# Kernel tuning notes

Measured on AMD Instinct MI355X. Metric: run time of the kernel, lower is better.

The kernel has to match this reference:

```python
import jax, jax.numpy as jnp
import numpy as np

B, T, C, H = 4, 2048, 1024, 16
D = C // H  # head_dim = 64
ROPE_BASE = 10000.0
EPS = 1e-6


def _rms_norm(x):
    return x / jnp.sqrt(jnp.mean(x * x, axis=-1, keepdims=True) + EPS)


def _rope_tables(t_len, d, dtype):
    inv_freq = 1.0 / (ROPE_BASE ** (jnp.arange(0, d, 2, dtype=jnp.float32) / d))
    t = jnp.arange(t_len, dtype=jnp.float32)
    freqs = jnp.outer(t, inv_freq)  # [T, D/2]
    return jnp.cos(freqs).astype(dtype)[None, None], jnp.sin(freqs).astype(dtype)[None, None]


def _apply_rotary(x, cos, sin):
    d = x.shape[-1] // 2
    x1, x2 = x[..., :d], x[..., d:]
    return jnp.concatenate([x1 * cos + x2 * sin, -x1 * sin + x2 * cos], axis=-1)


def setup_inputs() -> dict:
    key = jax.random.key(0)
    k1, k2, k3, k4, k5 = jax.random.split(key, 5)
    x = jax.random.normal(k1, (B, T, C), dtype=jnp.float32)
    Wqkv = jax.random.normal(k2, (C, 3 * C), dtype=jnp.float32) * 0.02
    bqkv = jax.random.normal(k3, (3 * C,), dtype=jnp.float32) * 0.02
    # NOTE: original zero-inits c_proj.weight; randomized here for a non-trivial baseline.
    Wproj = jax.random.normal(k4, (C, C), dtype=jnp.float32) * 0.02
    bproj = jax.random.normal(k5, (C,), dtype=jnp.float32) * 0.02
    lamb = jnp.float32(0.5)
    return {"x": x, "Wqkv": Wqkv, "bqkv": bqkv, "Wproj": Wproj, "bproj": bproj, "lamb": lamb}


def reference(x, Wqkv, bqkv, Wproj, bproj, lamb):
    b, t, c = x.shape
    qkv = x @ Wqkv + bqkv  # [B,T,3C]
    q, k, v = jnp.split(qkv, 3, axis=-1)
    # [B,T,C] -> [B,H,T,D]
    to_heads = lambda z: z.reshape(b, t, H, D).transpose(0, 2, 1, 3)
    query, key_, value = to_heads(q), to_heads(k), to_heads(v)
    # v1 defaults to value -> blend is identity, kept for faithfulness
    value = (1.0 - lamb) * value + lamb * value
    query = _rms_norm(query)
    key_ = _rms_norm(key_)
    cos, sin = _rope_tables(t, D, x.dtype)
    query = _apply_rotary(query, cos, sin)
    key_ = _apply_rotary(key_, cos, sin)
    # causal SDPA
    scale = 1.0 / jnp.sqrt(jnp.float32(D)).astype(x.dtype)
    scores = jnp.einsum('bhqd,bhkd->bhqk', query, key_) * scale
    causal = jnp.tril(jnp.ones((t, t), dtype=bool))
    scores = jnp.where(causal[None, None], scores, jnp.finfo(scores.dtype).min)
    probs = jax.nn.softmax(scores, axis=-1)
    attn = jnp.einsum('bhqk,bhkd->bhqd', probs, value)
    attn = attn.transpose(0, 2, 1, 3).reshape(b, t, c)
    out = attn @ Wproj + bproj
    return out, value
```

## Files before the change

kernel.cpp:

```cpp
#include <hip/hip_runtime.h>
#include <math.h>

#define B_   4
#define T_   2048
#define C_   1024
#define H_   16
#define D_   64
#define TC3  3072

typedef __attribute__((ext_vector_type(8))) short short8;
typedef __attribute__((ext_vector_type(4))) short short4b;
typedef __attribute__((ext_vector_type(8))) unsigned short ushortv8;
typedef __attribute__((ext_vector_type(4))) float f32x4;

__device__ __forceinline__ float bf2f(unsigned short u) {
  unsigned int x = ((unsigned int)u) << 16;
  float f; __builtin_memcpy(&f, &x, 4); return f;
}
__device__ __forceinline__ unsigned short f2bf(float f) {
  unsigned int x; __builtin_memcpy(&x, &f, 4);
  x += 0x7fff + ((x >> 16) & 1);
  return (unsigned short)(x >> 16);
}

#define MFMA32(a, b, c) __builtin_amdgcn_mfma_f32_16x16x32_bf16(a, b, c, 0, 0, 0)
#if __has_builtin(__builtin_amdgcn_mfma_f32_16x16x16_bf16)
#define MFMA16(a, b, c) __builtin_amdgcn_mfma_f32_16x16x16_bf16(a, b, c, 0, 0, 0)
#else
#define MFMA16(a, b, c) __builtin_amdgcn_mfma_f32_16x16x16bf16_1k(a, b, c, 0, 0, 0)
#endif

#define GLOAD_LDS(gp, lp) __builtin_amdgcn_global_load_lds( \
    (const __attribute__((address_space(1))) unsigned int*)(gp), \
    (__attribute__((address_space(3))) unsigned int*)(lp), 16, 0, 0)

__global__ __launch_bounds__(256)
void convert_bf16(const float* __restrict__ x, unsigned short* __restrict__ xb) {
  const size_t i = ((size_t)blockIdx.x * 256 + threadIdx.x) * 8;
  float4 f0 = *(const float4*)(x + i);
  float4 f1 = *(const float4*)(x + i + 4);
  ushortv8 u = { f2bf(f0.x), f2bf(f0.y), f2bf(f0.z), f2bf(f0.w),
                 f2bf(f1.x), f2bf(f1.y), f2bf(f1.z), f2bf(f1.w) };
  *(ushortv8*)(xb + i) = u;
}

__global__ __launch_bounds__(256)
void transpose_bf16(const float* __restrict__ W, unsigned short* __restrict__ WT,
                    int K, int N) {
  __shared__ float tile[64][65];
  const int k0 = blockIdx.y * 64, n0 = blockIdx.x * 64;
  const int r = threadIdx.x >> 4, c4 = (threadIdx.x & 15) * 4;
#pragma unroll
  for (int p = 0; p < 4; ++p) {
    int kk = p * 16 + r;
    float4 v = *(const float4*)(W + (size_t)(k0 + kk) * N + n0 + c4);
    tile[kk][c4 + 0] = v.x; tile[kk][c4 + 1] = v.y;
    tile[kk][c4 + 2] = v.z; tile[kk][c4 + 3] = v.w;
  }
  __syncthreads();
#pragma unroll
  for (int p = 0; p < 4; ++p) {
    int nn = p * 16 + r;
    ushort4 o = { f2bf(tile[c4 + 0][nn]), f2bf(tile[c4 + 1][nn]),
                  f2bf(tile[c4 + 2][nn]), f2bf(tile[c4 + 3][nn]) };
    *(ushort4*)(WT + (size_t)(n0 + nn) * K + k0 + c4) = o;
  }
}

template<bool OUT_BF16>
__global__ __launch_bounds__(256)
void gemm_mfma(const unsigned short* __restrict__ Ab,
               const unsigned short* __restrict__ Bt,
               const float* __restrict__ bias, void* __restrict__ Cv,
               int K, int lda, int ldb, int ldc) {
  __shared__ unsigned short As[128 * 64];
  __shared__ unsigned short Bs[128 * 64];
  const int tid = threadIdx.x;
  const int l = tid & 63, w = tid >> 6;
  const int m0 = blockIdx.y * 128, n0 = blockIdx.x * 128;
  const int wm = (w & 1) * 64, wn = (w >> 1) * 64;
  const int fr = l & 15, g = l >> 4;

  f32x4 acc[4][4];
#pragma unroll
  for (int i = 0; i < 4; ++i)
#pragma unroll
    for (int j = 0; j < 4; ++j) acc[i][j] = (f32x4)0.f;

  const int gr = l >> 3;
  const int gc = (l & 7) ^ gr;

  for (int kt = 0; kt < K; kt += 64) {
    __syncthreads();
#pragma unroll
    for (int q = 0; q < 4; ++q) {
      int rr = (w * 4 + q) * 8 + gr;
      GLOAD_LDS(Ab + (size_t)(m0 + rr) * lda + kt + gc * 8,
                &As[(w * 4 + q) * 512]);
      GLOAD_LDS(Bt + (size_t)(n0 + rr) * ldb + kt + gc * 8,
                &Bs[(w * 4 + q) * 512]);
    }
    __syncthreads();

#pragma unroll
    for (int s = 0; s < 2; ++s) {
      const int cofs = (((s * 4 + g) ^ (fr & 7)) << 3);
      short8 a[4], b[4];
#pragma unroll
      for (int i = 0; i < 4; ++i)
        a[i] = *(const short8*)&As[(wm + i * 16 + fr) * 64 + cofs];
#pragma unroll
      for (int j = 0; j < 4; ++j)
        b[j] = *(const short8*)&Bs[(wn + j * 16 + fr) * 64 + cofs];
#pragma unroll
      for (int i = 0; i < 4; ++i)
#pragma unroll
        for (int j = 0; j < 4; ++j)
          acc[i][j] = MFMA32(a[i], b[j], acc[i][j]);
    }
  }

#pragma unroll
  for (int j = 0; j < 4; ++j) {
    const int n = n0 + wn + j * 16 + fr;
    const float bv = bias[n];
#pragma unroll
    for (int i = 0; i < 4; ++i) {
#pragma unroll
      for (int rg = 0; rg < 4; ++rg) {
        const int m = m0 + wm + i * 16 + g * 4 + rg;
        float v = acc[i][j][rg] + bv;
        if (OUT_BF16) ((unsigned short*)Cv)[(size_t)m * ldc + n] = f2bf(v);
        else          ((float*)Cv)[(size_t)m * ldc + n] = v;
      }
    }
  }
}

__global__ __launch_bounds__(256)
void rmsrope_kernel(unsigned short* __restrict__ qkv,
                    const float* __restrict__ lambp,
                    float* __restrict__ valOut) {
  const int unit = blockIdx.x * 4 + (threadIdx.x >> 6);
  const int lane = threadIdx.x & 63;
  const int b = unit / (T_ * H_);
  const int rem = unit % (T_ * H_);
  const int t = rem / H_;
  const int h = rem % H_;
  const size_t base = (size_t)(b * T_ + t) * TC3;
  const float lamb = lambp[0];

  const int i = lane & 31;
  const float inv = __builtin_amdgcn_exp2f(-13.2877123795494f * (float)(2 * i)
                                           * (1.0f / 64.0f));
  const float ang = (float)t * inv;
  const float cs = cosf(ang);
  const float sn = sinf(ang);

  {
    const size_t idx = base + h * 64 + lane;
    float q = bf2f(qkv[idx]);
    float ss = q * q;
    ss += __shfl_xor(ss, 32); ss += __shfl_xor(ss, 16);
    ss += __shfl_xor(ss, 8);  ss += __shfl_xor(ss, 4);
    ss += __shfl_xor(ss, 2);  ss += __shfl_xor(ss, 1);
    float qn = q * (1.0f / sqrtf(ss * (1.0f / 64.0f) + 1e-6f));
    float part = __shfl_xor(qn, 32);
    float out = (lane < 32) ? (qn * cs + part * sn) : (qn * cs - part * sn);
    qkv[idx] = f2bf(out);
  }
  {
    const size_t idx = base + C_ + h * 64 + lane;
    float k = bf2f(qkv[idx]);
    float ss = k * k;
    ss += __shfl_xor(ss, 32); ss += __shfl_xor(ss, 16);
    ss += __shfl_xor(ss, 8);  ss += __shfl_xor(ss, 4);
    ss += __shfl_xor(ss, 2);  ss += __shfl_xor(ss, 1);
    float kn = k * (1.0f / sqrtf(ss * (1.0f / 64.0f) + 1e-6f));
    float part = __shfl_xor(kn, 32);
    float out = (lane < 32) ? (kn * cs + part * sn) : (kn * cs - part * sn);
    qkv[idx] = f2bf(out);
  }
  {
    float v = bf2f(qkv[base + 2 * C_ + h * 64 + lane]);
    float val = (1.0f - lamb) * v + lamb * v;
    valOut[(size_t)((b * H_ + h) * T_ + t) * D_ + lane] = val;
  }
}

__global__ __launch_bounds__(256)
void vtrans_kernel(const unsigned short* __restrict__ qkv,
                   const float* __restrict__ lambp,
                   unsigned short* __restrict__ vT) {
  __shared__ float tile[64][65];
  const int t0 = blockIdx.x * 64;
  const int head = blockIdx.y;
  const int b = head >> 4, h = head & 15;
  const float lamb = lambp[0];
  const int r = threadIdx.x >> 4, c4 = (threadIdx.x & 15) * 4;
#pragma unroll
  for (int p = 0; p < 4; ++p) {
    int tt = p * 16 + r;
    ushort4 raw = *(const ushort4*)(
        qkv + (size_t)(b * T_ + t0 + tt) * TC3 + 2 * C_ + h * 64 + c4);
    tile[tt][c4 + 0] = (1.f - lamb) * bf2f(raw.x) + lamb * bf2f(raw.x);
    tile[tt][c4 + 1] = (1.f - lamb) * bf2f(raw.y) + lamb * bf2f(raw.y);
    tile[tt][c4 + 2] = (1.f - lamb) * bf2f(raw.z) + lamb * bf2f(raw.z);
    tile[tt][c4 + 3] = (1.f - lamb) * bf2f(raw.w) + lamb * bf2f(raw.w);
  }
  __syncthreads();
#pragma unroll
  for (int p = 0; p < 4; ++p) {
    int d = p * 16 + r;
    ushort4 o = { f2bf(tile[c4 + 0][d]), f2bf(tile[c4 + 1][d]),
                  f2bf(tile[c4 + 2][d]), f2bf(tile[c4 + 3][d]) };
    *(ushort4*)(vT + ((size_t)head * D_ + d) * T_ + t0 + c4) = o;
  }
}

__global__ __launch_bounds__(256)
void flash_mfma(unsigned short* __restrict__ qkv,
                const unsigned short* __restrict__ vT) {
  __shared__ unsigned short Qs[128 * 64];
  __shared__ unsigned short Ks[64 * 64];
  __shared__ unsigned short Vs[64 * 64];

  const int z = blockIdx.z;
  const int xx = ((int)blockIdx.x + ((z >> 1) << 3)) & 15;
  const int qt = (z & 1) ? (15 - xx) : xx;
  const int b  = z;
  const int h  = blockIdx.y;

  const int tid = threadIdx.x;
  const int w = tid >> 6, l = tid & 63;
  const int fr = l & 15, quad = l >> 4;
  const int q0 = qt * 128;
  const int gr = l >> 3;
  const int gc = (l & 7) ^ gr;
  const int f8 = fr & 7;

#pragma unroll
  for (int s = 0; s < 4; ++s) {
    int row = w * 32 + s * 8 + gr;
    GLOAD_LDS(qkv + (size_t)(b * T_ + q0 + row) * TC3 + h * 64 + gc * 8,
              &Qs[(w * 32 + s * 8) * 64]);
  }
  __syncthreads();

  short8 qf[2][2];
#pragma unroll
  for (int kc = 0; kc < 2; ++kc) {
    const int cofs = (((kc * 4 + quad) ^ f8) << 3);
    qf[kc][0] = *(const short8*)&Qs[(w * 32 + fr) * 64 + cofs];
    qf[kc][1] = *(const short8*)&Qs[(w * 32 + 16 + fr) * 64 + cofs];
  }

  float l_pt[2] = {0.f, 0.f};
  f32x4 o[2][4];
#pragma unroll
  for (int i = 0; i < 2; ++i)
#pragma unroll
    for (int j = 0; j < 4; ++j) o[i][j] = (f32x4)0.f;

  const float SCL = 0.125f * 1.44269504088896f;
  const int nk = 2 * qt + 2;
  for (int kt = 0; kt < nk; ++kt) {
    const int k0 = kt * 64;
    __syncthreads();
#pragma unroll
    for (int s = 0; s < 2; ++s) {
      int row = w * 16 + s * 8;
      GLOAD_LDS(qkv + (size_t)(b * T_ + k0 + row + gr) * TC3 + C_ + h * 64 + gc * 8,
                &Ks[row * 64]);
      GLOAD_LDS(vT + ((size_t)(b * H_ + h) * D_ + row + gr) * T_ + k0 + gc * 8,
                &Vs[row * 64]);
    }
    __syncthreads();

    f32x4 st[2][4];
#pragma unroll
    for (int i = 0; i < 2; ++i)
#pragma unroll
      for (int j = 0; j < 4; ++j) st[i][j] = (f32x4)0.f;

#pragma unroll
    for (int kc = 0; kc < 2; ++kc) {
      const int cofs = (((kc * 4 + quad) ^ f8) << 3);
#pragma unroll
      for (int j = 0; j < 4; ++j) {
        short8 kf = *(const short8*)&Ks[(j * 16 + fr) * 64 + cofs];
        st[0][j] = MFMA32(kf, qf[kc][0], st[0][j]);
        st[1][j] = MFMA32(kf, qf[kc][1], st[1][j]);
      }
    }

    short4b pa[2][4];
#pragma unroll
    for (int i = 0; i < 2; ++i) {
      const int qg = q0 + w * 32 + i * 16 + fr;
#pragma unroll
      for (int j = 0; j < 4; ++j) {
        const int kg = k0 + j * 16 + quad * 4;
#pragma unroll
        for (int r = 0; r < 4; ++r) {
          float arg = st[i][j][r] * SCL;
          if (kg + r > qg) arg = -INFINITY;
          float p = __builtin_amdgcn_exp2f(arg);
          l_pt[i] += p;
          st[i][j][r] = p;
        }
        pa[i][j] = (short4b){ (short)f2bf(st[i][j][0]), (short)f2bf(st[i][j][1]),
                              (short)f2bf(st[i][j][2]), (short)f2bf(st[i][j][3]) };
      }
    }

#pragma unroll
    for (int c = 0; c < 4; ++c) {
      const int vofs = ((((c * 2 + (quad >> 1)) ^ f8) << 3) + (quad & 1) * 4);
#pragma unroll
      for (int jd = 0; jd < 4; ++jd) {
        short4b vf = *(const short4b*)&Vs[(jd * 16 + fr) * 64 + vofs];
        o[0][jd] = MFMA16(pa[0][c], vf, o[0][jd]);
        o[1][jd] = MFMA16(pa[1][c], vf, o[1][jd]);
      }
    }
  }

#pragma unroll
  for (int i = 0; i < 2; ++i) {
    float lv = l_pt[i];
    lv += __shfl_xor(lv, 16);
    lv += __shfl_xor(lv, 32);
    float inv = 1.0f / lv;
    float invq[4];
#pragma unroll
    for (int r = 0; r < 4; ++r) invq[r] = __shfl(inv, quad * 4 + r);
#pragma unroll
    for (int jd = 0; jd < 4; ++jd) {
      const int d = jd * 16 + fr;
#pragma unroll
      for (int r = 0; r < 4; ++r) {
        const int row = q0 + w * 32 + i * 16 + quad * 4 + r;
        qkv[(size_t)(b * T_ + row) * TC3 + 2 * C_ + h * 64 + d] =
            f2bf(o[i][jd][r] * invq[r]);
      }
    }
  }
}

extern "C" void kernel_launch(void* const* d_in, const int* in_sizes, int n_in,
                              void* d_out, int out_size, void* d_ws, size_t ws_size,
                              hipStream_t stream) {
  const float* x     = (const float*)d_in[0];
  const float* Wqkv  = (const float*)d_in[1];
  const float* bqkv  = (const float*)d_in[2];
  const float* Wproj = (const float*)d_in[3];
  const float* bproj = (const float*)d_in[4];
  const float* lamb  = (const float*)d_in[5];

  float* out     = (float*)d_out;
  float* val_out = out + (size_t)B_ * T_ * C_;

  unsigned short* qkvb   = (unsigned short*)d_ws;
  unsigned short* WqkvT  = qkvb + (size_t)B_ * T_ * TC3;
  unsigned short* WprojT = WqkvT + (size_t)TC3 * C_;
  unsigned short* vT     = WprojT + (size_t)C_ * C_;
  unsigned short* xb     = vT + (size_t)B_ * H_ * D_ * T_;

  convert_bf16<<<dim3((B_ * T_ * C_) / 2048), 256, 0, stream>>>(x, xb);
  transpose_bf16<<<dim3(TC3 / 64, C_ / 64), 256, 0, stream>>>(Wqkv, WqkvT, C_, TC3);
  transpose_bf16<<<dim3(C_ / 64, C_ / 64), 256, 0, stream>>>(Wproj, WprojT, C_, C_);

  gemm_mfma<true><<<dim3(TC3 / 128, (B_ * T_) / 128), 256, 0, stream>>>(
      xb, WqkvT, bqkv, qkvb, C_, C_, C_, TC3);

  rmsrope_kernel<<<dim3((B_ * T_ * H_) / 4), 256, 0, stream>>>(qkvb, lamb, val_out);

  vtrans_kernel<<<dim3(T_ / 64, B_ * H_), 256, 0, stream>>>(qkvb, lamb, vT);

  flash_mfma<<<dim3(T_ / 128, H_, B_), 256, 0, stream>>>(qkvb, vT);

  gemm_mfma<false><<<dim3(C_ / 128, (B_ * T_) / 128), 256, 0, stream>>>(
      qkvb + 2 * C_, WprojT, bproj, out, C_, TC3, C_, C_);
}
```

Before: 332.1 us.

## Pair complementary causal query tiles per block and move value output to vtrans

Each flash-attention block now handles two query tiles, qa and 15-qa, so every block does the same amount of causal work. The K/V tiles loaded for the longer tile are reused by the shorter one, and the causal mask is applied only on the last two diagonal key tiles through a template specialization. The fp32 value output write moves from the rmsrope kernel into the vtrans kernel as vectorized float4 stores. The grid halves to 512 blocks, and doubled Q registers and LDS may reduce occupancy.

```diff
diff --git a/kernel.cpp b/kernel.cpp
--- a/kernel.cpp
+++ b/kernel.cpp
@@ -138,9 +138,7 @@
 }
 
 __global__ __launch_bounds__(256)
-void rmsrope_kernel(unsigned short* __restrict__ qkv,
-                    const float* __restrict__ lambp,
-                    float* __restrict__ valOut) {
+void rmsrope_kernel(unsigned short* __restrict__ qkv) {
   const int unit = blockIdx.x * 4 + (threadIdx.x >> 6);
   const int lane = threadIdx.x & 63;
   const int b = unit / (T_ * H_);
@@ -148,7 +146,6 @@
   const int t = rem / H_;
   const int h = rem % H_;
   const size_t base = (size_t)(b * T_ + t) * TC3;
-  const float lamb = lambp[0];
 
   const int i = lane & 31;
   const float inv = __builtin_amdgcn_exp2f(-13.2877123795494f * (float)(2 * i)
@@ -181,17 +178,13 @@
     float out = (lane < 32) ? (kn * cs + part * sn) : (kn * cs - part * sn);
     qkv[idx] = f2bf(out);
   }
-  {
-    float v = bf2f(qkv[base + 2 * C_ + h * 64 + lane]);
-    float val = (1.0f - lamb) * v + lamb * v;
-    valOut[(size_t)((b * H_ + h) * T_ + t) * D_ + lane] = val;
-  }
 }
 
 __global__ __launch_bounds__(256)
 void vtrans_kernel(const unsigned short* __restrict__ qkv,
                    const float* __restrict__ lambp,
-                   unsigned short* __restrict__ vT) {
+                   unsigned short* __restrict__ vT,
+                   float* __restrict__ valOut) {
   __shared__ float tile[64][65];
   const int t0 = blockIdx.x * 64;
   const int head = blockIdx.y;
@@ -203,10 +196,14 @@
     int tt = p * 16 + r;
     ushort4 raw = *(const ushort4*)(
         qkv + (size_t)(b * T_ + t0 + tt) * TC3 + 2 * C_ + h * 64 + c4);
-    tile[tt][c4 + 0] = (1.f - lamb) * bf2f(raw.x) + lamb * bf2f(raw.x);
-    tile[tt][c4 + 1] = (1.f - lamb) * bf2f(raw.y) + lamb * bf2f(raw.y);
-    tile[tt][c4 + 2] = (1.f - lamb) * bf2f(raw.z) + lamb * bf2f(raw.z);
-    tile[tt][c4 + 3] = (1.f - lamb) * bf2f(raw.w) + lamb * bf2f(raw.w);
+    float4 f;
+    f.x = (1.f - lamb) * bf2f(raw.x) + lamb * bf2f(raw.x);
+    f.y = (1.f - lamb) * bf2f(raw.y) + lamb * bf2f(raw.y);
+    f.z = (1.f - lamb) * bf2f(raw.z) + lamb * bf2f(raw.z);
+    f.w = (1.f - lamb) * bf2f(raw.w) + lamb * bf2f(raw.w);
+    tile[tt][c4 + 0] = f.x; tile[tt][c4 + 1] = f.y;
+    tile[tt][c4 + 2] = f.z; tile[tt][c4 + 3] = f.w;
+    *(float4*)(valOut + ((size_t)head * T_ + t0 + tt) * D_ + c4) = f;
   }
   __syncthreads();
 #pragma unroll
@@ -218,114 +215,67 @@
   }
 }
 
-__global__ __launch_bounds__(256)
-void flash_mfma(unsigned short* __restrict__ qkv,
-                const unsigned short* __restrict__ vT) {
-  __shared__ unsigned short Qs[128 * 64];
-  __shared__ unsigned short Ks[64 * 64];
-  __shared__ unsigned short Vs[64 * 64];
-
-  const int z = blockIdx.z;
-  const int xx = ((int)blockIdx.x + ((z >> 1) << 3)) & 15;
-  const int qt = (z & 1) ? (15 - xx) : xx;
-  const int b  = z;
-  const int h  = blockIdx.y;
-
-  const int tid = threadIdx.x;
-  const int w = tid >> 6, l = tid & 63;
-  const int fr = l & 15, quad = l >> 4;
-  const int q0 = qt * 128;
-  const int gr = l >> 3;
-  const int gc = (l & 7) ^ gr;
-  const int f8 = fr & 7;
-
-#pragma unroll
-  for (int s = 0; s < 4; ++s) {
-    int row = w * 32 + s * 8 + gr;
-    GLOAD_LDS(qkv + (size_t)(b * T_ + q0 + row) * TC3 + h * 64 + gc * 8,
-              &Qs[(w * 32 + s * 8) * 64]);
-  }
-  __syncthreads();
-
-  short8 qf[2][2];
+#define SCL_ (0.125f * 1.44269504088896f)
+
+template<bool MASKED>
+__device__ __forceinline__ void attn_tile(
+    const unsigned short* __restrict__ Ks,
+    const unsigned short* __restrict__ Vs,
+    const short8 (&qf)[2][2], int qrow0 , int k0,
+    int fr, int quad, int f8,
+    float (&l_pt)[2], f32x4 (&o)[2][4]) {
+  f32x4 st[2][4];
+#pragma unroll
+  for (int i = 0; i < 2; ++i)
+#pragma unroll
+    for (int j = 0; j < 4; ++j) st[i][j] = (f32x4)0.f;
+
 #pragma unroll
   for (int kc = 0; kc < 2; ++kc) {
     const int cofs = (((kc * 4 + quad) ^ f8) << 3);
-    qf[kc][0] = *(const short8*)&Qs[(w * 32 + fr) * 64 + cofs];
-    qf[kc][1] = *(const short8*)&Qs[(w * 32 + 16 + fr) * 64 + cofs];
-  }
-
-  float l_pt[2] = {0.f, 0.f};
-  f32x4 o[2][4];
-#pragma unroll
-  for (int i = 0; i < 2; ++i)
-#pragma unroll
-    for (int j = 0; j < 4; ++j) o[i][j] = (f32x4)0.f;
-
-  const float SCL = 0.125f * 1.44269504088896f;
-  const int nk = 2 * qt + 2;
-  for (int kt = 0; kt < nk; ++kt) {
-    const int k0 = kt * 64;
-    __syncthreads();
-#pragma unroll
-    for (int s = 0; s < 2; ++s) {
-      int row = w * 16 + s * 8;
-      GLOAD_LDS(qkv + (size_t)(b * T_ + k0 + row + gr) * TC3 + C_ + h * 64 + gc * 8,
-                &Ks[row * 64]);
-      GLOAD_LDS(vT + ((size_t)(b * H_ + h) * D_ + row + gr) * T_ + k0 + gc * 8,
-                &Vs[row * 64]);
-    }
-    __syncthreads();
-
-    f32x4 st[2][4];
-#pragma unroll
-    for (int i = 0; i < 2; ++i)
-#pragma unroll
-      for (int j = 0; j < 4; ++j) st[i][j] = (f32x4)0.f;
-
-#pragma unroll
-    for (int kc = 0; kc < 2; ++kc) {
-      const int cofs = (((kc * 4 + quad) ^ f8) << 3);
-#pragma unroll
-      for (int j = 0; j < 4; ++j) {
-        short8 kf = *(const short8*)&Ks[(j * 16 + fr) * 64 + cofs];
-        st[0][j] = MFMA32(kf, qf[kc][0], st[0][j]);
-        st[1][j] = MFMA32(kf, qf[kc][1], st[1][j]);
+#pragma unroll
+    for (int j = 0; j < 4; ++j) {
+      short8 kf = *(const short8*)&Ks[(j * 16 + fr) * 64 + cofs];
+      st[0][j] = MFMA32(kf, qf[kc][0], st[0][j]);
+      st[1][j] = MFMA32(kf, qf[kc][1], st[1][j]);
+    }
+  }
+
+  short4b pa[2][4];
+#pragma unroll
+  for (int i = 0; i < 2; ++i) {
+    const int qg = qrow0 + i * 16 + fr;
+#pragma unroll
+    for (int j = 0; j < 4; ++j) {
+      const int kg = k0 + j * 16 + quad * 4;
+#pragma unroll
+      for (int r = 0; r < 4; ++r) {
+        float arg = st[i][j][r] * SCL_;
+        if (MASKED) { if (kg + r > qg) arg = -INFINITY; }
+        float p = __builtin_amdgcn_exp2f(arg);
+        l_pt[i] += p;
+        st[i][j][r] = p;
       }
-    }
-
-    short4b pa[2][4];
-#pragma unroll
-    for (int i = 0; i < 2; ++i) {
-      const int qg = q0 + w * 32 + i * 16 + fr;
-#pragma unroll
-      for (int j = 0; j < 4; ++j) {
-        const int kg = k0 + j * 16 + quad * 4;
-#pragma unroll
-        for (int r = 0; r < 4; ++r) {
-          float arg = st[i][j][r] * SCL;
-          if (kg + r > qg) arg = -INFINITY;
-          float p = __builtin_amdgcn_exp2f(arg);
-          l_pt[i] += p;
-          st[i][j][r] = p;
-        }
-        pa[i][j] = (short4b){ (short)f2bf(st[i][j][0]), (short)f2bf(st[i][j][1]),
-                              (short)f2bf(st[i][j][2]), (short)f2bf(st[i][j][3]) };
-      }
-    }
-
-#pragma unroll
-    for (int c = 0; c < 4; ++c) {
-      const int vofs = ((((c * 2 + (quad >> 1)) ^ f8) << 3) + (quad & 1) * 4);
-#pragma unroll
-      for (int jd = 0; jd < 4; ++jd) {
-        short4b vf = *(const short4b*)&Vs[(jd * 16 + fr) * 64 + vofs];
-        o[0][jd] = MFMA16(pa[0][c], vf, o[0][jd]);
-        o[1][jd] = MFMA16(pa[1][c], vf, o[1][jd]);
-      }
-    }
-  }
-
+      pa[i][j] = (short4b){ (short)f2bf(st[i][j][0]), (short)f2bf(st[i][j][1]),
+                            (short)f2bf(st[i][j][2]), (short)f2bf(st[i][j][3]) };
+    }
+  }
+
+#pragma unroll
+  for (int c = 0; c < 4; ++c) {
+    const int vofs = ((((c * 2 + (quad >> 1)) ^ f8) << 3) + (quad & 1) * 4);
+#pragma unroll
+    for (int jd = 0; jd < 4; ++jd) {
+      short4b vf = *(const short4b*)&Vs[(jd * 16 + fr) * 64 + vofs];
+      o[0][jd] = MFMA16(pa[0][c], vf, o[0][jd]);
+      o[1][jd] = MFMA16(pa[1][c], vf, o[1][jd]);
+    }
+  }
+}
+
+__device__ __forceinline__ void attn_store(
+    unsigned short* __restrict__ qkv, int bT, int h, int qrow0,
+    int fr, int quad, float (&l_pt)[2], f32x4 (&o)[2][4]) {
 #pragma unroll
   for (int i = 0; i < 2; ++i) {
     float lv = l_pt[i];
@@ -340,12 +290,93 @@
       const int d = jd * 16 + fr;
 #pragma unroll
       for (int r = 0; r < 4; ++r) {
-        const int row = q0 + w * 32 + i * 16 + quad * 4 + r;
-        qkv[(size_t)(b * T_ + row) * TC3 + 2 * C_ + h * 64 + d] =
+        const int row = qrow0 + i * 16 + quad * 4 + r;
+        qkv[(size_t)(bT + row) * TC3 + 2 * C_ + h * 64 + d] =
             f2bf(o[i][jd][r] * invq[r]);
       }
     }
   }
+}
+
+__global__ __launch_bounds__(256)
+void flash_mfma(unsigned short* __restrict__ qkv,
+                const unsigned short* __restrict__ vT) {
+  __shared__ unsigned short Qs[2][128 * 64];
+  __shared__ unsigned short Ks[64 * 64];
+  __shared__ unsigned short Vs[64 * 64];
+
+  const int qa = blockIdx.x;
+  const int qb = 15 - qa;
+  const int b  = blockIdx.z;
+  const int h  = blockIdx.y;
+  const int bT = b * T_;
+
+  const int tid = threadIdx.x;
+  const int w = tid >> 6, l = tid & 63;
+  const int fr = l & 15, quad = l >> 4;
+  const int gr = l >> 3;
+  const int gc = (l & 7) ^ gr;
+  const int f8 = fr & 7;
+
+#pragma unroll
+  for (int s = 0; s < 4; ++s) {
+    int row = w * 32 + s * 8 + gr;
+    GLOAD_LDS(qkv + (size_t)(bT + qa * 128 + row) * TC3 + h * 64 + gc * 8,
+              &Qs[0][(w * 32 + s * 8) * 64]);
+    GLOAD_LDS(qkv + (size_t)(bT + qb * 128 + row) * TC3 + h * 64 + gc * 8,
+              &Qs[1][(w * 32 + s * 8) * 64]);
+  }
+  __syncthreads();
+
+  short8 qfa[2][2], qfb[2][2];
+#pragma unroll
+  for (int kc = 0; kc < 2; ++kc) {
+    const int cofs = (((kc * 4 + quad) ^ f8) << 3);
+    qfa[kc][0] = *(const short8*)&Qs[0][(w * 32 + fr) * 64 + cofs];
+    qfa[kc][1] = *(const short8*)&Qs[0][(w * 32 + 16 + fr) * 64 + cofs];
+    qfb[kc][0] = *(const short8*)&Qs[1][(w * 32 + fr) * 64 + cofs];
+    qfb[kc][1] = *(const short8*)&Qs[1][(w * 32 + 16 + fr) * 64 + cofs];
+  }
+
+  float la[2] = {0.f, 0.f}, lb[2] = {0.f, 0.f};
+  f32x4 oa[2][4], ob[2][4];
+#pragma unroll
+  for (int i = 0; i < 2; ++i)
+#pragma unroll
+    for (int j = 0; j < 4; ++j) { oa[i][j] = (f32x4)0.f; ob[i][j] = (f32x4)0.f; }
+
+  const int nka = 2 * qa + 2;
+  const int nkb = 2 * qb + 2;
+  const int qra = qa * 128 + w * 32;
+  const int qrb = qb * 128 + w * 32;
+
+  for (int kt = 0; kt < nkb; ++kt) {
+    const int k0 = kt * 64;
+    __syncthreads();
+#pragma unroll
+    for (int s = 0; s < 2; ++s) {
+      int row = w * 16 + s * 8;
+      GLOAD_LDS(qkv + (size_t)(bT + k0 + row + gr) * TC3 + C_ + h * 64 + gc * 8,
+                &Ks[row * 64]);
+      GLOAD_LDS(vT + ((size_t)(b * H_ + h) * D_ + row + gr) * T_ + k0 + gc * 8,
+                &Vs[row * 64]);
+    }
+    __syncthreads();
+
+    if (kt < nka) {
+      if (kt >= nka - 2)
+        attn_tile<true >(Ks, Vs, qfa, qra, k0, fr, quad, f8, la, oa);
+      else
+        attn_tile<false>(Ks, Vs, qfa, qra, k0, fr, quad, f8, la, oa);
+    }
+    if (kt >= nkb - 2)
+      attn_tile<true >(Ks, Vs, qfb, qrb, k0, fr, quad, f8, lb, ob);
+    else
+      attn_tile<false>(Ks, Vs, qfb, qrb, k0, fr, quad, f8, lb, ob);
+  }
+
+  attn_store(qkv, bT, h, qra, fr, quad, la, oa);
+  attn_store(qkv, bT, h, qrb, fr, quad, lb, ob);
 }
 
 extern "C" void kernel_launch(void* const* d_in, const int* in_sizes, int n_in,
@@ -374,11 +405,11 @@
   gemm_mfma<true><<<dim3(TC3 / 128, (B_ * T_) / 128), 256, 0, stream>>>(
       xb, WqkvT, bqkv, qkvb, C_, C_, C_, TC3);
 
-  rmsrope_kernel<<<dim3((B_ * T_ * H_) / 4), 256, 0, stream>>>(qkvb, lamb, val_out);
-
-  vtrans_kernel<<<dim3(T_ / 64, B_ * H_), 256, 0, stream>>>(qkvb, lamb, vT);
-
-  flash_mfma<<<dim3(T_ / 128, H_, B_), 256, 0, stream>>>(qkvb, vT);
+  rmsrope_kernel<<<dim3((B_ * T_ * H_) / 4), 256, 0, stream>>>(qkvb);
+
+  vtrans_kernel<<<dim3(T_ / 64, B_ * H_), 256, 0, stream>>>(qkvb, lamb, vT, val_out);
+
+  flash_mfma<<<dim3(8, H_, B_), 256, 0, stream>>>(qkvb, vT);
 
   gemm_mfma<false><<<dim3(C_ / 128, (B_ * T_) / 128), 256, 0, stream>>>(
       qkvb + 2 * C_, WprojT, bproj, out, C_, TC3, C_, C_);
```

After: 341.2 us. +2.7%, slower.
